# Kernel tuning notes

Hardware: AMD Instinct MI355X
Metric: run time of the kernel (lower is better)

Reference implementation:

```python
import jax, jax.numpy as jnp
import numpy as np

B, T, N, D = 2, 16, 512, 256
HID, HEADS = 256, 8
HD = HID // HEADS // 2  # 16
SCALE = HD ** -0.5
LAMBDA_INIT = 0.8 - 0.6 * float(np.exp(-0.3 * (2 - 1)))  # layer_idx = 2
LN_EPS = 1e-5


def setup_inputs() -> dict:
    key = jax.random.key(0)
    ks = jax.random.split(key, 8)
    return {
        "x": jax.random.normal(ks[0], (B, T, N, D), dtype=jnp.float32),
        "Wq": jax.random.normal(ks[1], (D, HID), dtype=jnp.float32) * (D ** -0.5),
        "Wk": jax.random.normal(ks[2], (D, HID), dtype=jnp.float32) * (D ** -0.5),
        "Wv": jax.random.normal(ks[3], (D, HID), dtype=jnp.float32) * (D ** -0.5),
        "lq1": jax.random.normal(ks[4], (HD,), dtype=jnp.float32) * 0.1,
        "lk1": jax.random.normal(ks[5], (HD,), dtype=jnp.float32) * 0.1,
        "lq2": jax.random.normal(ks[6], (HD,), dtype=jnp.float32) * 0.1,
        "lk2": jax.random.normal(ks[7], (HD,), dtype=jnp.float32) * 0.1,
        "ln_gamma": jnp.ones((2 * HD,), dtype=jnp.float32),
        "ln_beta": jnp.zeros((2 * HD,), dtype=jnp.float32),
    }


def _attn_pair(q, k, v1, v2):
    # q,k,v*: [BT, N, H, HD]; shared softmax applied to both value halves
    p = jax.nn.softmax(jnp.einsum('bnhd,bmhd->bhnm', q, k) * SCALE, axis=-1)
    o1 = jnp.einsum('bhnm,bmhd->bnhd', p, v1)
    o2 = jnp.einsum('bhnm,bmhd->bnhd', p, v2)
    return jnp.concatenate([o1, o2], axis=-1)  # [BT, N, H, 2*HD]


def reference(x, Wq, Wk, Wv, lq1, lk1, lq2, lk2, ln_gamma, ln_beta):
    b, t, n, d = x.shape
    # 1x1 Conv2d over channel dim == per-token linear projection
    q = jnp.einsum('btnd,dh->btnh', x, Wq).reshape(b * t, n, HEADS, 2 * HD)
    k = jnp.einsum('btnd,dh->btnh', x, Wk).reshape(b * t, n, HEADS, 2 * HD)
    v = jnp.einsum('btnd,dh->btnh', x, Wv).reshape(b * t, n, HEADS, 2 * HD)
    q1, q2 = jnp.split(q, 2, axis=-1)
    k1, k2 = jnp.split(k, 2, axis=-1)
    v1, v2 = jnp.split(v, 2, axis=-1)
    attn1 = _attn_pair(q1, k1, v1, v2)
    attn2 = _attn_pair(q2, k2, v1, v2)
    lam = jnp.exp(jnp.sum(lq1 * lk1)) - jnp.exp(jnp.sum(lq2 * lk2)) + LAMBDA_INIT
    y = attn1 - lam * attn2  # [BT, N, H, 2*HD]
    mu = jnp.mean(y, axis=-1, keepdims=True)
    var = jnp.mean(jnp.square(y - mu), axis=-1, keepdims=True)
    y = (y - mu) * jax.lax.rsqrt(var + LN_EPS) * ln_gamma + ln_beta
    y = y * (1.0 - LAMBDA_INIT)
    return y.reshape(b, t, n, HEADS * 2 * HD)
```

## Files before the change

### kernel.cpp

```cpp
#include <hip/hip_runtime.h>
#include <cmath>

typedef unsigned short u16;
typedef unsigned int   u32;
typedef __attribute__((ext_vector_type(8))) short short8;
typedef __attribute__((ext_vector_type(4))) float f32x4;

constexpr int BT    = 32;
constexpr int NTOK  = 512;
constexpr int DIM   = 256;
constexpr int HID   = 256;
constexpr int M_ROWS = BT * NTOK;
constexpr int HM     = M_ROWS * 32;
constexpr size_t TENS = (size_t)M_ROWS * HID;
constexpr float LAMBDA_INIT  = 0.35550906759096927f;
constexpr float ONE_MINUS_LI = 0.6444909324090307f;
constexpr float LN_EPS = 1e-5f;
constexpr float QSCALE = 0.36067376022224085f;

#define MFMA16(a, b, c) __builtin_amdgcn_mfma_f32_16x16x32_bf16((a), (b), (c), 0, 0, 0)

__device__ __forceinline__ u16 f2bf(float f) {
    u32 u = __float_as_uint(f);
    return (u16)((u + 0x7FFFu + ((u >> 16) & 1u)) >> 16);
}

__device__ __forceinline__ float fexp2(float x) {
#if defined(__has_builtin) && __has_builtin(__builtin_amdgcn_exp2f)
    return __builtin_amdgcn_exp2f(x);
#else
    return exp2f(x);
#endif
}

__device__ __forceinline__ u32 pack_bf16(float a, float b) {
    u32 ua = __float_as_uint(a) + 0x8000u;
    u32 ub = __float_as_uint(b) + 0x8000u;
    return __builtin_amdgcn_perm(ub, ua, 0x07060302u);
}

__global__ __launch_bounds__(256) void prep_w(const float* __restrict__ Wq,
                                              const float* __restrict__ Wk,
                                              const float* __restrict__ Wv,
                                              u16* __restrict__ Wt) {
    const float* W = (blockIdx.z == 0) ? Wq : (blockIdx.z == 1) ? Wk : Wv;
    u16* dst = Wt + (size_t)blockIdx.z * 65536;
    __shared__ float T[64][65];
    const int k0 = blockIdx.x * 64, n0 = blockIdx.y * 64;
    const int tr = threadIdx.x >> 4;
    const int tc = threadIdx.x & 15;
    #pragma unroll
    for (int i = 0; i < 4; ++i) {
        int row = tr + i * 16;
        float4 v = *(const float4*)&W[(size_t)(k0 + row) * HID + n0 + tc * 4];
        T[row][tc * 4 + 0] = v.x; T[row][tc * 4 + 1] = v.y;
        T[row][tc * 4 + 2] = v.z; T[row][tc * 4 + 3] = v.w;
    }
    __syncthreads();
    #pragma unroll
    for (int i = 0; i < 4; ++i) {
        int n = tr + i * 16;
        int k4 = tc * 4;
        uint2 pk;
        pk.x = (u32)f2bf(T[k4 + 0][n]) | ((u32)f2bf(T[k4 + 1][n]) << 16);
        pk.y = (u32)f2bf(T[k4 + 2][n]) | ((u32)f2bf(T[k4 + 3][n]) << 16);
        *(uint2*)&dst[(size_t)(n0 + n) * DIM + k0 + k4] = pk;
    }
}

__global__ __launch_bounds__(256, 3) void proj_kernel(
    const float* __restrict__ x, const u16* __restrict__ Wt,
    u16* __restrict__ Qh, u16* __restrict__ Kh, u16* __restrict__ Vh)
{
    __shared__ u16 As[64 * 72];
    __shared__ u16 Bs[3][64 * 72];

    const int tid  = threadIdx.x;
    const int m0   = blockIdx.x * 64;
    const int n0   = blockIdx.y * 64;
    const int lane = tid & 63;
    const int wv   = tid >> 6;
    const int q16  = lane & 15;
    const int quad = lane >> 4;
    const int mw   = (wv >> 1) * 32;
    const int nw   = (wv & 1) * 32;

    const int sr = tid >> 2;
    const int sc = (tid & 3) * 16;

    f32x4 acc[3][4];
    #pragma unroll
    for (int z = 0; z < 3; ++z)
        #pragma unroll
        for (int t = 0; t < 4; ++t)
            acc[z][t] = (f32x4){0.f, 0.f, 0.f, 0.f};

    for (int kk = 0; kk < DIM; kk += 64) {
        {
            const float4* xs = (const float4*)&x[(size_t)(m0 + sr) * DIM + kk + sc];
            float4 g0 = xs[0], g1 = xs[1], g2 = xs[2], g3 = xs[3];
            uint4 o0, o1;
            o0.x = (u32)f2bf(g0.x) | ((u32)f2bf(g0.y) << 16);
            o0.y = (u32)f2bf(g0.z) | ((u32)f2bf(g0.w) << 16);
            o0.z = (u32)f2bf(g1.x) | ((u32)f2bf(g1.y) << 16);
            o0.w = (u32)f2bf(g1.z) | ((u32)f2bf(g1.w) << 16);
            o1.x = (u32)f2bf(g2.x) | ((u32)f2bf(g2.y) << 16);
            o1.y = (u32)f2bf(g2.z) | ((u32)f2bf(g2.w) << 16);
            o1.z = (u32)f2bf(g3.x) | ((u32)f2bf(g3.y) << 16);
            o1.w = (u32)f2bf(g3.z) | ((u32)f2bf(g3.w) << 16);
            *(uint4*)&As[sr * 72 + sc]     = o0;
            *(uint4*)&As[sr * 72 + sc + 8] = o1;
        }
        #pragma unroll
        for (int z = 0; z < 3; ++z) {
            const uint4* ws4 = (const uint4*)&Wt[(size_t)z * 65536 + (size_t)(n0 + sr) * DIM + kk + sc];
            *(uint4*)&Bs[z][sr * 72 + sc]     = ws4[0];
            *(uint4*)&Bs[z][sr * 72 + sc + 8] = ws4[1];
        }
        __syncthreads();
        #pragma unroll
        for (int kc = 0; kc < 2; ++kc) {
            short8 a0 = *(const short8*)&As[(mw +      q16) * 72 + kc * 32 + quad * 8];
            short8 a1 = *(const short8*)&As[(mw + 16 + q16) * 72 + kc * 32 + quad * 8];
            #pragma unroll
            for (int z = 0; z < 3; ++z) {
                short8 b0 = *(const short8*)&Bs[z][(nw +      q16) * 72 + kc * 32 + quad * 8];
                short8 b1 = *(const short8*)&Bs[z][(nw + 16 + q16) * 72 + kc * 32 + quad * 8];
                acc[z][0] = MFMA16(a0, b0, acc[z][0]);
                acc[z][1] = MFMA16(a0, b1, acc[z][1]);
                acc[z][2] = MFMA16(a1, b0, acc[z][2]);
                acc[z][3] = MFMA16(a1, b1, acc[z][3]);
            }
        }
        __syncthreads();
    }

    const int hcol = (n0 + nw) >> 5;
    #pragma unroll
    for (int z = 0; z < 3; ++z) {
        u16* C = (z == 0) ? Qh : (z == 1) ? Kh : Vh;
        u16* base = C + (size_t)hcol * HM;
        const float s = (z == 0) ? QSCALE : 1.0f;
        #pragma unroll
        for (int r = 0; r < 4; ++r) {
            const int row = m0 + mw + quad * 4 + r;
            base[(size_t)row * 32 + q16]             = f2bf(acc[z][0][r] * s);
            base[(size_t)row * 32 + q16 + 16]        = f2bf(acc[z][1][r] * s);
            base[(size_t)(row + 16) * 32 + q16]      = f2bf(acc[z][2][r] * s);
            base[(size_t)(row + 16) * 32 + q16 + 16] = f2bf(acc[z][3][r] * s);
        }
    }
}

__global__ __launch_bounds__(256, 3) void attn_kernel(
    const u16* __restrict__ Qh, const u16* __restrict__ Kh, const u16* __restrict__ Vh,
    const float* __restrict__ lq1, const float* __restrict__ lk1,
    const float* __restrict__ lq2, const float* __restrict__ lk2,
    const float* __restrict__ gamma, const float* __restrict__ beta,
    float* __restrict__ out)
{
    __shared__ u16 Ks[256 * 40];
    __shared__ u16 Vts[32 * 264];
    __shared__ u16 Pbuf[4][2][16 * 40];

    const int qh  = blockIdx.x;
    const int h   = blockIdx.y;
    const int bt  = blockIdx.z;
    const int tid = threadIdx.x;
    const int lane = tid & 63;
    const int wv   = tid >> 6;
    const int q16  = lane & 15;
    const int quad = lane >> 4;

    float sa = 0.f, sb = 0.f;
    #pragma unroll
    for (int d = 0; d < 16; ++d) { sa += lq1[d] * lk1[d]; sb += lq2[d] * lk2[d]; }
    const float lam = __expf(sa) - __expf(sb) + LAMBDA_INIT;

    short8 qv[2];
    #pragma unroll
    for (int qbi = 0; qbi < 2; ++qbi) {
        const int qrow = bt * NTOK + qh * 128 + (qbi * 4 + wv) * 16 + q16;
        qv[qbi] = *(const short8*)(Qh + (size_t)h * HM + (size_t)qrow * 32 + quad * 8);
    }

    const short8 z8 = {0, 0, 0, 0, 0, 0, 0, 0};
    const f32x4  z4 = {0.f, 0.f, 0.f, 0.f};

    f32x4 o1lo[2], o1hi[2], o2lo[2], o2hi[2];
    #pragma unroll
    for (int qbi = 0; qbi < 2; ++qbi) {
        o1lo[qbi] = z4; o1hi[qbi] = z4; o2lo[qbi] = z4; o2hi[qbi] = z4;
    }
    float l1[2] = {0.f, 0.f}, l2[2] = {0.f, 0.f};

    u16* P1 = &Pbuf[wv][0][0];
    u16* P2 = &Pbuf[wv][1][0];

    for (int chunk = 0; chunk < 2; ++chunk) {
        if (chunk) __syncthreads();
        {
            const uint4* src = (const uint4*)(Kh + (size_t)h * HM +
                                (size_t)(bt * NTOK + chunk * 256 + tid) * 32);
            uint4* dst = (uint4*)&Ks[tid * 40];
            dst[0] = src[0]; dst[1] = src[1]; dst[2] = src[2]; dst[3] = src[3];
        }
        if (tid < 128) {
            const int j0 = tid * 2;
            const u16* v0 = Vh + (size_t)h * HM + (size_t)(bt * NTOK + chunk * 256 + j0) * 32;
            union U { uint4 q[4]; u32 w[16]; } ra, rb;
            #pragma unroll
            for (int i = 0; i < 4; ++i) {
                ra.q[i] = ((const uint4*)v0)[i];
                rb.q[i] = ((const uint4*)(v0 + 32))[i];
            }
            #pragma unroll
            for (int w = 0; w < 16; ++w) {
                u32 lo = __builtin_amdgcn_perm(rb.w[w], ra.w[w], 0x05040100u);
                u32 hi = __builtin_amdgcn_perm(rb.w[w], ra.w[w], 0x07060302u);
                *(u32*)&Vts[(2 * w)     * 264 + j0] = lo;
                *(u32*)&Vts[(2 * w + 1) * 264 + j0] = hi;
            }
        }
        __syncthreads();

        #pragma unroll
        for (int qbi = 0; qbi < 2; ++qbi) {
            const short8 A1 = (lane < 32) ? qv[qbi] : z8;
            const short8 A2 = (lane < 32) ? z8 : qv[qbi];
            for (int kc = 0; kc < 8; ++kc) {
                #pragma unroll
                for (int sub = 0; sub < 2; ++sub) {
                    const int key0 = kc * 32 + sub * 16;
                    short8 kf = *(const short8*)&Ks[(key0 + q16) * 40 + quad * 8];
                    f32x4 s1 = MFMA16(kf, A1, z4);
                    f32x4 s2 = MFMA16(kf, A2, z4);
                    float p0 = fexp2(s1[0]), p1 = fexp2(s1[1]);
                    float p2 = fexp2(s1[2]), p3 = fexp2(s1[3]);
                    l1[qbi] += (p0 + p1) + (p2 + p3);
                    uint2 w1; w1.x = pack_bf16(p0, p1); w1.y = pack_bf16(p2, p3);
                    *(uint2*)&P1[q16 * 40 + sub * 16 + quad * 4] = w1;
                    float r0 = fexp2(s2[0]), r1 = fexp2(s2[1]);
                    float r2 = fexp2(s2[2]), r3 = fexp2(s2[3]);
                    l2[qbi] += (r0 + r1) + (r2 + r3);
                    uint2 w2; w2.x = pack_bf16(r0, r1); w2.y = pack_bf16(r2, r3);
                    *(uint2*)&P2[q16 * 40 + sub * 16 + quad * 4] = w2;
                }
                short8 pf1 = *(const short8*)&P1[q16 * 40 + quad * 8];
                short8 pf2 = *(const short8*)&P2[q16 * 40 + quad * 8];
                short8 vlo = *(const short8*)&Vts[q16        * 264 + kc * 32 + quad * 8];
                short8 vhi = *(const short8*)&Vts[(16 + q16) * 264 + kc * 32 + quad * 8];
                o1lo[qbi] = MFMA16(pf1, vlo, o1lo[qbi]);
                o1hi[qbi] = MFMA16(pf1, vhi, o1hi[qbi]);
                o2lo[qbi] = MFMA16(pf2, vlo, o2lo[qbi]);
                o2hi[qbi] = MFMA16(pf2, vhi, o2hi[qbi]);
            }
        }
    }

    const float g_lo = gamma[q16],      g_hi = gamma[16 + q16];
    const float b_lo = beta[q16],       b_hi = beta[16 + q16];

    #pragma unroll
    for (int qbi = 0; qbi < 2; ++qbi) {
        float a = l1[qbi], b = l2[qbi];
        a += __shfl_xor(a, 16); a += __shfl_xor(a, 32);
        b += __shfl_xor(b, 16); b += __shfl_xor(b, 32);
        const float inv1 = 1.0f / a;
        const float inv2 = 1.0f / b;
        #pragma unroll
        for (int r = 0; r < 4; ++r) {
            const float i1 = __shfl(inv1, quad * 4 + r);
            const float i2 = __shfl(inv2, quad * 4 + r);
            const float ylo = o1lo[qbi][r] * i1 - lam * (o2lo[qbi][r] * i2);
            const float yhi = o1hi[qbi][r] * i1 - lam * (o2hi[qbi][r] * i2);

            float s  = ylo + yhi;
            float s2 = ylo * ylo + yhi * yhi;
            #pragma unroll
            for (int off = 1; off < 16; off <<= 1) {
                s  += __shfl_xor(s,  off);
                s2 += __shfl_xor(s2, off);
            }
            const float mu   = s * (1.0f / 32.0f);
            const float var  = s2 * (1.0f / 32.0f) - mu * mu;
            const float rstd = rsqrtf(var + LN_EPS);

            const int row = bt * NTOK + qh * 128 + (qbi * 4 + wv) * 16 + quad * 4 + r;
            float* orow = out + (size_t)row * HID + h * 32;
            orow[q16]      = ((ylo - mu) * rstd * g_lo + b_lo) * ONE_MINUS_LI;
            orow[16 + q16] = ((yhi - mu) * rstd * g_hi + b_hi) * ONE_MINUS_LI;
        }
    }
}

extern "C" void kernel_launch(void* const* d_in, const int* in_sizes, int n_in,
                              void* d_out, int out_size, void* d_ws, size_t ws_size,
                              hipStream_t stream) {
    const float* x   = (const float*)d_in[0];
    const float* Wq  = (const float*)d_in[1];
    const float* Wk  = (const float*)d_in[2];
    const float* Wv  = (const float*)d_in[3];
    const float* lq1 = (const float*)d_in[4];
    const float* lk1 = (const float*)d_in[5];
    const float* lq2 = (const float*)d_in[6];
    const float* lk2 = (const float*)d_in[7];
    const float* gam = (const float*)d_in[8];
    const float* bet = (const float*)d_in[9];
    float* out = (float*)d_out;

    u16* ws = (u16*)d_ws;
    u16* Wt = ws;
    u16* Qh = Wt + 3 * 65536;
    u16* Kh = Qh + TENS;
    u16* Vh = Kh + TENS;

    hipLaunchKernelGGL(prep_w, dim3(4, 4, 3), dim3(256), 0, stream, Wq, Wk, Wv, Wt);
    hipLaunchKernelGGL(proj_kernel, dim3(M_ROWS / 64, HID / 64), dim3(256), 0, stream,
                       x, Wt, Qh, Kh, Vh);
    hipLaunchKernelGGL(attn_kernel, dim3(4, 8, 32), dim3(256), 0, stream,
                       Qh, Kh, Vh, lq1, lk1, lq2, lk2, gam, bet, out);
}
```

Before: 134.3 us.

## Use 32x32 MFMA in attention, prefetch projection tiles, swap grid order

```diff
diff --git a/kernel.cpp b/kernel.cpp
--- a/kernel.cpp
+++ b/kernel.cpp
@@ -3,8 +3,9 @@
 
 typedef unsigned short u16;
 typedef unsigned int   u32;
-typedef __attribute__((ext_vector_type(8))) short short8;
-typedef __attribute__((ext_vector_type(4))) float f32x4;
+typedef __attribute__((ext_vector_type(8)))  short short8;
+typedef __attribute__((ext_vector_type(4)))  float f32x4;
+typedef __attribute__((ext_vector_type(16))) float f32x16;
 
 constexpr int BT    = 32;
 constexpr int NTOK  = 512;
@@ -19,6 +20,7 @@
 constexpr float QSCALE = 0.36067376022224085f;
 
 #define MFMA16(a, b, c) __builtin_amdgcn_mfma_f32_16x16x32_bf16((a), (b), (c), 0, 0, 0)
+#define MFMA32(a, b, c) __builtin_amdgcn_mfma_f32_32x32x16_bf16((a), (b), (c), 0, 0, 0)
 
 __device__ __forceinline__ u16 f2bf(float f) {
     u32 u = __float_as_uint(f);
@@ -33,10 +35,8 @@
 #endif
 }
 
-__device__ __forceinline__ u32 pack_bf16(float a, float b) {
-    u32 ua = __float_as_uint(a) + 0x8000u;
-    u32 ub = __float_as_uint(b) + 0x8000u;
-    return __builtin_amdgcn_perm(ub, ua, 0x07060302u);
+__device__ __forceinline__ u32 pack_trunc(float a, float b) {
+    return __builtin_amdgcn_perm(__float_as_uint(b), __float_as_uint(a), 0x07060302u);
 }
 
 __global__ __launch_bounds__(256) void prep_w(const float* __restrict__ Wq,
@@ -76,8 +76,8 @@
     __shared__ u16 Bs[3][64 * 72];
 
     const int tid  = threadIdx.x;
-    const int m0   = blockIdx.x * 64;
-    const int n0   = blockIdx.y * 64;
+    const int n0   = blockIdx.x * 64;
+    const int m0   = blockIdx.y * 64;
     const int lane = tid & 63;
     const int wv   = tid >> 6;
     const int q16  = lane & 15;
@@ -95,29 +95,50 @@
         for (int t = 0; t < 4; ++t)
             acc[z][t] = (f32x4){0.f, 0.f, 0.f, 0.f};
 
-    for (int kk = 0; kk < DIM; kk += 64) {
+    float4 ga[4];
+    uint4  gb[3][2];
+    {
+        const float4* xs = (const float4*)&x[(size_t)(m0 + sr) * DIM + sc];
+        ga[0] = xs[0]; ga[1] = xs[1]; ga[2] = xs[2]; ga[3] = xs[3];
+        #pragma unroll
+        for (int z = 0; z < 3; ++z) {
+            const uint4* ws4 = (const uint4*)&Wt[(size_t)z * 65536 + (size_t)(n0 + sr) * DIM + sc];
+            gb[z][0] = ws4[0]; gb[z][1] = ws4[1];
+        }
+    }
+
+    for (int it = 0; it < 4; ++it) {
         {
-            const float4* xs = (const float4*)&x[(size_t)(m0 + sr) * DIM + kk + sc];
-            float4 g0 = xs[0], g1 = xs[1], g2 = xs[2], g3 = xs[3];
             uint4 o0, o1;
-            o0.x = (u32)f2bf(g0.x) | ((u32)f2bf(g0.y) << 16);
-            o0.y = (u32)f2bf(g0.z) | ((u32)f2bf(g0.w) << 16);
-            o0.z = (u32)f2bf(g1.x) | ((u32)f2bf(g1.y) << 16);
-            o0.w = (u32)f2bf(g1.z) | ((u32)f2bf(g1.w) << 16);
-            o1.x = (u32)f2bf(g2.x) | ((u32)f2bf(g2.y) << 16);
-            o1.y = (u32)f2bf(g2.z) | ((u32)f2bf(g2.w) << 16);
-            o1.z = (u32)f2bf(g3.x) | ((u32)f2bf(g3.y) << 16);
-            o1.w = (u32)f2bf(g3.z) | ((u32)f2bf(g3.w) << 16);
+            o0.x = (u32)f2bf(ga[0].x) | ((u32)f2bf(ga[0].y) << 16);
+            o0.y = (u32)f2bf(ga[0].z) | ((u32)f2bf(ga[0].w) << 16);
+            o0.z = (u32)f2bf(ga[1].x) | ((u32)f2bf(ga[1].y) << 16);
+            o0.w = (u32)f2bf(ga[1].z) | ((u32)f2bf(ga[1].w) << 16);
+            o1.x = (u32)f2bf(ga[2].x) | ((u32)f2bf(ga[2].y) << 16);
+            o1.y = (u32)f2bf(ga[2].z) | ((u32)f2bf(ga[2].w) << 16);
+            o1.z = (u32)f2bf(ga[3].x) | ((u32)f2bf(ga[3].y) << 16);
+            o1.w = (u32)f2bf(ga[3].z) | ((u32)f2bf(ga[3].w) << 16);
             *(uint4*)&As[sr * 72 + sc]     = o0;
             *(uint4*)&As[sr * 72 + sc + 8] = o1;
-        }
-        #pragma unroll
-        for (int z = 0; z < 3; ++z) {
-            const uint4* ws4 = (const uint4*)&Wt[(size_t)z * 65536 + (size_t)(n0 + sr) * DIM + kk + sc];
-            *(uint4*)&Bs[z][sr * 72 + sc]     = ws4[0];
-            *(uint4*)&Bs[z][sr * 72 + sc + 8] = ws4[1];
+            #pragma unroll
+            for (int z = 0; z < 3; ++z) {
+                *(uint4*)&Bs[z][sr * 72 + sc]     = gb[z][0];
+                *(uint4*)&Bs[z][sr * 72 + sc + 8] = gb[z][1];
+            }
         }
         __syncthreads();
+
+        if (it < 3) {
+            const int kk = (it + 1) * 64;
+            const float4* xs = (const float4*)&x[(size_t)(m0 + sr) * DIM + kk + sc];
+            ga[0] = xs[0]; ga[1] = xs[1]; ga[2] = xs[2]; ga[3] = xs[3];
+            #pragma unroll
+            for (int z = 0; z < 3; ++z) {
+                const uint4* ws4 = (const uint4*)&Wt[(size_t)z * 65536 + (size_t)(n0 + sr) * DIM + kk + sc];
+                gb[z][0] = ws4[0]; gb[z][1] = ws4[1];
+            }
+        }
+
         #pragma unroll
         for (int kc = 0; kc < 2; ++kc) {
             short8 a0 = *(const short8*)&As[(mw +      q16) * 72 + kc * 32 + quad * 8];
@@ -144,10 +165,10 @@
         #pragma unroll
         for (int r = 0; r < 4; ++r) {
             const int row = m0 + mw + quad * 4 + r;
-            base[(size_t)row * 32 + q16]             = f2bf(acc[z][0][r] * s);
-            base[(size_t)row * 32 + q16 + 16]        = f2bf(acc[z][1][r] * s);
-            base[(size_t)(row + 16) * 32 + q16]      = f2bf(acc[z][2][r] * s);
-            base[(size_t)(row + 16) * 32 + q16 + 16] = f2bf(acc[z][3][r] * s);
+            base[(size_t)row * 32 + q16]              = f2bf(acc[z][0][r] * s);
+            base[(size_t)row * 32 + q16 + 16]         = f2bf(acc[z][1][r] * s);
+            base[(size_t)(row + 16) * 32 + q16]       = f2bf(acc[z][2][r] * s);
+            base[(size_t)(row + 16) * 32 + q16 + 16]  = f2bf(acc[z][3][r] * s);
         }
     }
 }
@@ -161,7 +182,7 @@
 {
     __shared__ u16 Ks[256 * 40];
     __shared__ u16 Vts[32 * 264];
-    __shared__ u16 Pbuf[4][2][16 * 40];
+    __shared__ u16 Pb[4][32 * 40];
 
     const int qh  = blockIdx.x;
     const int h   = blockIdx.y;
@@ -169,33 +190,23 @@
     const int tid = threadIdx.x;
     const int lane = tid & 63;
     const int wv   = tid >> 6;
-    const int q16  = lane & 15;
-    const int quad = lane >> 4;
+    const int l31  = lane & 31;
+    const int hi   = lane >> 5;
 
     float sa = 0.f, sb = 0.f;
     #pragma unroll
     for (int d = 0; d < 16; ++d) { sa += lq1[d] * lk1[d]; sb += lq2[d] * lk2[d]; }
     const float lam = __expf(sa) - __expf(sb) + LAMBDA_INIT;
 
-    short8 qv[2];
-    #pragma unroll
-    for (int qbi = 0; qbi < 2; ++qbi) {
-        const int qrow = bt * NTOK + qh * 128 + (qbi * 4 + wv) * 16 + q16;
-        qv[qbi] = *(const short8*)(Qh + (size_t)h * HM + (size_t)qrow * 32 + quad * 8);
-    }
-
-    const short8 z8 = {0, 0, 0, 0, 0, 0, 0, 0};
-    const f32x4  z4 = {0.f, 0.f, 0.f, 0.f};
-
-    f32x4 o1lo[2], o1hi[2], o2lo[2], o2hi[2];
-    #pragma unroll
-    for (int qbi = 0; qbi < 2; ++qbi) {
-        o1lo[qbi] = z4; o1hi[qbi] = z4; o2lo[qbi] = z4; o2hi[qbi] = z4;
-    }
-    float l1[2] = {0.f, 0.f}, l2[2] = {0.f, 0.f};
-
-    u16* P1 = &Pbuf[wv][0][0];
-    u16* P2 = &Pbuf[wv][1][0];
+    const int qbase = bt * NTOK + qh * 128 + wv * 32;
+    const u16* qrowp = Qh + (size_t)h * HM + (size_t)(qbase + l31) * 32 + hi * 8;
+    const short8 B1 = *(const short8*)qrowp;
+    const short8 B2 = *(const short8*)(qrowp + 16);
+
+    const f32x16 z16 = {0.f,0.f,0.f,0.f,0.f,0.f,0.f,0.f,0.f,0.f,0.f,0.f,0.f,0.f,0.f,0.f};
+    f32x16 O1 = z16, O2 = z16;
+    float l1 = 0.f, l2 = 0.f;
+    u16* P = &Pb[wv][0];
 
     for (int chunk = 0; chunk < 2; ++chunk) {
         if (chunk) __syncthreads();
@@ -217,80 +228,85 @@
             #pragma unroll
             for (int w = 0; w < 16; ++w) {
                 u32 lo = __builtin_amdgcn_perm(rb.w[w], ra.w[w], 0x05040100u);
-                u32 hi = __builtin_amdgcn_perm(rb.w[w], ra.w[w], 0x07060302u);
+                u32 hi2 = __builtin_amdgcn_perm(rb.w[w], ra.w[w], 0x07060302u);
                 *(u32*)&Vts[(2 * w)     * 264 + j0] = lo;
-                *(u32*)&Vts[(2 * w + 1) * 264 + j0] = hi;
+                *(u32*)&Vts[(2 * w + 1) * 264 + j0] = hi2;
             }
         }
         __syncthreads();
 
-        #pragma unroll
-        for (int qbi = 0; qbi < 2; ++qbi) {
-            const short8 A1 = (lane < 32) ? qv[qbi] : z8;
-            const short8 A2 = (lane < 32) ? z8 : qv[qbi];
-            for (int kc = 0; kc < 8; ++kc) {
-                #pragma unroll
-                for (int sub = 0; sub < 2; ++sub) {
-                    const int key0 = kc * 32 + sub * 16;
-                    short8 kf = *(const short8*)&Ks[(key0 + q16) * 40 + quad * 8];
-                    f32x4 s1 = MFMA16(kf, A1, z4);
-                    f32x4 s2 = MFMA16(kf, A2, z4);
-                    float p0 = fexp2(s1[0]), p1 = fexp2(s1[1]);
-                    float p2 = fexp2(s1[2]), p3 = fexp2(s1[3]);
-                    l1[qbi] += (p0 + p1) + (p2 + p3);
-                    uint2 w1; w1.x = pack_bf16(p0, p1); w1.y = pack_bf16(p2, p3);
-                    *(uint2*)&P1[q16 * 40 + sub * 16 + quad * 4] = w1;
-                    float r0 = fexp2(s2[0]), r1 = fexp2(s2[1]);
-                    float r2 = fexp2(s2[2]), r3 = fexp2(s2[3]);
-                    l2[qbi] += (r0 + r1) + (r2 + r3);
-                    uint2 w2; w2.x = pack_bf16(r0, r1); w2.y = pack_bf16(r2, r3);
-                    *(uint2*)&P2[q16 * 40 + sub * 16 + quad * 4] = w2;
-                }
-                short8 pf1 = *(const short8*)&P1[q16 * 40 + quad * 8];
-                short8 pf2 = *(const short8*)&P2[q16 * 40 + quad * 8];
-                short8 vlo = *(const short8*)&Vts[q16        * 264 + kc * 32 + quad * 8];
-                short8 vhi = *(const short8*)&Vts[(16 + q16) * 264 + kc * 32 + quad * 8];
-                o1lo[qbi] = MFMA16(pf1, vlo, o1lo[qbi]);
-                o1hi[qbi] = MFMA16(pf1, vhi, o1hi[qbi]);
-                o2lo[qbi] = MFMA16(pf2, vlo, o2lo[qbi]);
-                o2hi[qbi] = MFMA16(pf2, vhi, o2hi[qbi]);
-            }
-        }
-    }
-
-    const float g_lo = gamma[q16],      g_hi = gamma[16 + q16];
-    const float b_lo = beta[q16],       b_hi = beta[16 + q16];
-
-    #pragma unroll
-    for (int qbi = 0; qbi < 2; ++qbi) {
-        float a = l1[qbi], b = l2[qbi];
-        a += __shfl_xor(a, 16); a += __shfl_xor(a, 32);
-        b += __shfl_xor(b, 16); b += __shfl_xor(b, 32);
-        const float inv1 = 1.0f / a;
-        const float inv2 = 1.0f / b;
-        #pragma unroll
-        for (int r = 0; r < 4; ++r) {
-            const float i1 = __shfl(inv1, quad * 4 + r);
-            const float i2 = __shfl(inv2, quad * 4 + r);
-            const float ylo = o1lo[qbi][r] * i1 - lam * (o2lo[qbi][r] * i2);
-            const float yhi = o1hi[qbi][r] * i1 - lam * (o2hi[qbi][r] * i2);
-
-            float s  = ylo + yhi;
-            float s2 = ylo * ylo + yhi * yhi;
-            #pragma unroll
-            for (int off = 1; off < 16; off <<= 1) {
-                s  += __shfl_xor(s,  off);
-                s2 += __shfl_xor(s2, off);
-            }
-            const float mu   = s * (1.0f / 32.0f);
-            const float var  = s2 * (1.0f / 32.0f) - mu * mu;
-            const float rstd = rsqrtf(var + LN_EPS);
-
-            const int row = bt * NTOK + qh * 128 + (qbi * 4 + wv) * 16 + quad * 4 + r;
-            float* orow = out + (size_t)row * HID + h * 32;
-            orow[q16]      = ((ylo - mu) * rstd * g_lo + b_lo) * ONE_MINUS_LI;
-            orow[16 + q16] = ((yhi - mu) * rstd * g_hi + b_hi) * ONE_MINUS_LI;
-        }
+        for (int kc = 0; kc < 8; ++kc) {
+            const u16* krow = &Ks[(kc * 32 + l31) * 40 + hi * 8];
+            const short8 A1 = *(const short8*)krow;
+            const short8 A2 = *(const short8*)(krow + 16);
+            const u16* vrow = &Vts[l31 * 264 + kc * 32 + hi * 8];
+            const short8 Vt0 = *(const short8*)vrow;
+            const short8 Vt1 = *(const short8*)(vrow + 16);
+
+            f32x16 S = MFMA32(A1, B1, z16);
+            #pragma unroll
+            for (int rg = 0; rg < 4; ++rg) {
+                float e0 = fexp2(S[4 * rg + 0]);
+                float e1 = fexp2(S[4 * rg + 1]);
+                float e2 = fexp2(S[4 * rg + 2]);
+                float e3 = fexp2(S[4 * rg + 3]);
+                l1 += (e0 + e1) + (e2 + e3);
+                uint2 w; w.x = pack_trunc(e0, e1); w.y = pack_trunc(e2, e3);
+                *(uint2*)&P[l31 * 40 + rg * 8 + hi * 4] = w;
+            }
+            {
+                const short8 P0  = *(const short8*)&P[l31 * 40 + hi * 8];
+                const short8 P1f = *(const short8*)&P[l31 * 40 + 16 + hi * 8];
+                O1 = MFMA32(P0,  Vt0, O1);
+                O1 = MFMA32(P1f, Vt1, O1);
+            }
+            S = MFMA32(A2, B2, z16);
+            #pragma unroll
+            for (int rg = 0; rg < 4; ++rg) {
+                float e0 = fexp2(S[4 * rg + 0]);
+                float e1 = fexp2(S[4 * rg + 1]);
+                float e2 = fexp2(S[4 * rg + 2]);
+                float e3 = fexp2(S[4 * rg + 3]);
+                l2 += (e0 + e1) + (e2 + e3);
+                uint2 w; w.x = pack_trunc(e0, e1); w.y = pack_trunc(e2, e3);
+                *(uint2*)&P[l31 * 40 + rg * 8 + hi * 4] = w;
+            }
+            {
+                const short8 P0  = *(const short8*)&P[l31 * 40 + hi * 8];
+                const short8 P1f = *(const short8*)&P[l31 * 40 + 16 + hi * 8];
+                O2 = MFMA32(P0,  Vt0, O2);
+                O2 = MFMA32(P1f, Vt1, O2);
+            }
+        }
+    }
+
+    l1 += __shfl_xor(l1, 32);
+    l2 += __shfl_xor(l2, 32);
+    const float i1base = 1.0f / l1;
+    const float i2base = 1.0f / l2;
+    const float g = gamma[l31];
+    const float bc = beta[l31];
+
+    #pragma unroll
+    for (int r = 0; r < 16; ++r) {
+        const int qloc = (r & 3) + 8 * (r >> 2) + 4 * hi;
+        const float i1 = __shfl(i1base, qloc);
+        const float i2 = __shfl(i2base, qloc);
+        float y = O1[r] * i1 - lam * (O2[r] * i2);
+
+        float s  = y;
+        float s2 = y * y;
+        #pragma unroll
+        for (int off = 1; off < 32; off <<= 1) {
+            s  += __shfl_xor(s,  off);
+            s2 += __shfl_xor(s2, off);
+        }
+        const float mu   = s * (1.0f / 32.0f);
+        const float var  = s2 * (1.0f / 32.0f) - mu * mu;
+        const float rstd = rsqrtf(var + LN_EPS);
+
+        const int row = qbase + qloc;
+        out[(size_t)row * HID + h * 32 + l31] = ((y - mu) * rstd * g + bc) * ONE_MINUS_LI;
     }
 }
 
@@ -316,7 +332,7 @@
     u16* Vh = Kh + TENS;
 
     hipLaunchKernelGGL(prep_w, dim3(4, 4, 3), dim3(256), 0, stream, Wq, Wk, Wv, Wt);
-    hipLaunchKernelGGL(proj_kernel, dim3(M_ROWS / 64, HID / 64), dim3(256), 0, stream,
+    hipLaunchKernelGGL(proj_kernel, dim3(HID / 64, M_ROWS / 64), dim3(256), 0, stream,
                        x, Wt, Qh, Kh, Vh);
     hipLaunchKernelGGL(attn_kernel, dim3(4, 8, 32), dim3(256), 0, stream,
                        Qh, Kh, Vh, lq1, lk1, lq2, lk2, gam, bet, out);
```

Result: slower. 157.4 us (+17.2%).
